# Performance work log

Hardware: AMD Instinct MI355X
Metric: run time of the kernel (lower is better)

## Reference

```python
import jax, jax.numpy as jnp
import numpy as np

N, E, B = 10000, 20000, 400
ND, ED, D = 32, 16, 64


def setup_inputs() -> dict:
    key = jax.random.key(0)
    ks = jax.random.split(key, 32)

    def lin(k, out_d, in_d):
        kw, kb = jax.random.split(k)
        s = 1.0 / np.sqrt(in_d)
        return (jax.random.uniform(kw, (out_d, in_d), jnp.float32, -s, s),
                jax.random.uniform(kb, (out_d,), jnp.float32, -s, s))

    W_in, b_in = lin(ks[0], D, ND)
    W_e1, b_e1 = lin(ks[1], D, ED)
    W_e2, b_e2 = lin(ks[2], D * D, D)
    b_conv = jax.random.uniform(ks[3], (D,), jnp.float32, -1/8.0, 1/8.0)
    W_ih, b_ih = lin(ks[4], 3 * D, D)
    W_hh, b_hh = lin(ks[5], 3 * D, D)
    W_ih_l, b_ih_l = lin(ks[6], 4 * D, 2 * D)
    W_hh_l, b_hh_l = lin(ks[7], 4 * D, D)
    W_o1, b_o1 = lin(ks[8], D, 2 * D)
    W_o2, b_o2 = lin(ks[9], 1, D)

    x = jax.random.normal(ks[10], (N, ND), jnp.float32)
    edge_attr = jax.random.normal(ks[11], (E, ED), jnp.float32)
    edge_index = jax.random.randint(ks[12], (2, E), 0, N, jnp.int64)
    batch = jnp.sort(jax.random.randint(ks[13], (N,), 0, B, jnp.int64))

    return dict(x=x, edge_attr=edge_attr,
                W_in=W_in, b_in=b_in, W_e1=W_e1, b_e1=b_e1, W_e2=W_e2, b_e2=b_e2,
                b_conv=b_conv, W_ih=W_ih, b_ih=b_ih, W_hh=W_hh, b_hh=b_hh,
                W_ih_l=W_ih_l, b_ih_l=b_ih_l, W_hh_l=W_hh_l, b_hh_l=b_hh_l,
                W_o1=W_o1, b_o1=b_o1, W_o2=W_o2, b_o2=b_o2,
                edge_index=edge_index, batch=batch)


def reference(x, edge_attr, W_in, b_in, W_e1, b_e1, W_e2, b_e2, b_conv,
              W_ih, b_ih, W_hh, b_hh, W_ih_l, b_ih_l, W_hh_l, b_hh_l,
              W_o1, b_o1, W_o2, b_o2, edge_index, batch):
    src, dst = edge_index[0], edge_index[1]

    # in_linear
    out = jax.nn.relu(x @ W_in.T + b_in)            # [N, D]
    h = out                                          # GRU hidden (layer=1, seq=1)

    # edge-conditioned weights: MLP(edge_attr) -> [E, D, D]
    ew = (jax.nn.relu(edge_attr @ W_e1.T + b_e1) @ W_e2.T + b_e2).reshape(E, D, D)
    cnt = jnp.maximum(jax.ops.segment_sum(jnp.ones((E,), x.dtype), dst, N), 1.0)

    for _ in range(3):
        # NNConv: gather src nodes, per-edge matmul, scatter-mean to dst, + bias
        msg = jnp.einsum('ed,edf->ef', out[src], ew)                 # [E, D]
        agg = jax.ops.segment_sum(msg, dst, N) / cnt[:, None] + b_conv
        m = jax.nn.relu(agg)
        # GRU cell (torch gate order r, z, n)
        gi = m @ W_ih.T + b_ih
        gh = h @ W_hh.T + b_hh
        i_r, i_z, i_n = jnp.split(gi, 3, axis=-1)
        h_r, h_z, h_n = jnp.split(gh, 3, axis=-1)
        r = jax.nn.sigmoid(i_r + h_r)
        z = jax.nn.sigmoid(i_z + h_z)
        n = jnp.tanh(i_n + r * h_n)
        h = (1.0 - z) * n + z * h
        out = h

    # Set2Set pooling, processing_steps=3
    q_star = jnp.zeros((B, 2 * D), x.dtype)
    hl = jnp.zeros((B, D), x.dtype)
    cl = jnp.zeros((B, D), x.dtype)
    for _ in range(3):
        g = q_star @ W_ih_l.T + b_ih_l + hl @ W_hh_l.T + b_hh_l
        gi_, gf_, gg_, go_ = jnp.split(g, 4, axis=-1)   # torch order i,f,g,o
        cl = jax.nn.sigmoid(gf_) * cl + jax.nn.sigmoid(gi_) * jnp.tanh(gg_)
        hl = jax.nn.sigmoid(go_) * jnp.tanh(cl)
        q = hl                                           # [B, D]
        e = jnp.sum(out * q[batch], axis=-1)             # [N]
        mmax = jax.ops.segment_max(e, batch, B)
        a = jnp.exp(e - mmax[batch])
        a = a / jax.ops.segment_sum(a, batch, B)[batch]
        r_ = jax.ops.segment_sum(a[:, None] * out, batch, B)  # [B, D]
        q_star = jnp.concatenate([q, r_], axis=-1)

    o = jax.nn.relu(q_star @ W_o1.T + b_o1) @ W_o2.T + b_o2
    return o.reshape(-1)
```

## Files before the change

### kernel.cpp

```cpp
#include <hip/hip_runtime.h>
#include <math.h>


#define Nn 10000
#define Ee 20000
#define Bb 400
#define KSTEPS 130
#define S2S_CHUNK 1024

#define FILL_A (Nn * 64)
#define FILL_B (KSTEPS * 4096)
#define FILL_C (4 * 2 * 16 * 64 * 8)

typedef __attribute__((ext_vector_type(8))) short bf16x8_t;
typedef __attribute__((ext_vector_type(4))) float f32x4_t;

__device__ __forceinline__ float sigmoidf_(float x) { return 1.f / (1.f + expf(-x)); }

__device__ __forceinline__ void split8(const float* p, bf16x8_t& Ahi_, bf16x8_t& Alo_) {
    union { bf16x8_t v; unsigned u[4]; } hi, lo;
#pragma unroll
    for (int ii = 0; ii < 4; ++ii) {
        float pa = p[2 * ii], pb = p[2 * ii + 1];
        unsigned ua = __float_as_uint(pa), ub = __float_as_uint(pb);
        hi.u[ii] = (ua >> 16) | (ub & 0xFFFF0000u);
        float la = pa - __uint_as_float(ua & 0xFFFF0000u);
        float lb = pb - __uint_as_float(ub & 0xFFFF0000u);
        lo.u[ii] = (__float_as_uint(la) >> 16) | (__float_as_uint(lb) & 0xFFFF0000u);
    }
    Ahi_ = hi.v; Alo_ = lo.v;
}

__global__ __launch_bounds__(256) void k_fill(const float* __restrict__ x,
                                              const float* __restrict__ Win,
                                              const float* __restrict__ bin,
                                              const float* __restrict__ W2,
                                              const float* __restrict__ b2,
                                              const float* __restrict__ Wih,
                                              const float* __restrict__ Whh,
                                              float* __restrict__ out,
                                              unsigned short* __restrict__ Bfat,
                                              unsigned short* __restrict__ Wg) {
    int idx = blockIdx.x * 256 + threadIdx.x;
    if (idx < FILL_A) {
        int n = idx >> 6, j = idx & 63;
        const float* xr = x + n * 32;
        const float* w = Win + j * 32;
        float acc = bin[j];
#pragma unroll
        for (int k = 0; k < 32; ++k) acc += xr[k] * w[k];
        out[idx] = fmaxf(acc, 0.f);
        return;
    }
    idx -= FILL_A;
    if (idx < FILL_B) {
        int i  = idx & 7;
        int l  = (idx >> 3) & 63;
        int nq = (idx >> 9) & 3;
        int h  = (idx >> 11) & 1;
        int ks = idx >> 12;
        int kap = ks * 32 + (l >> 4) * 8 + i;
        int f = nq * 16 + (l & 15);
        float w;
        if (kap < 4096) {
            int q = kap >> 6, d = kap & 63;
            w = W2[(size_t)(d * 64 + f) * 64 + q];
        } else {
            int d = kap - 4096;
            w = b2[d * 64 + f];
        }
        unsigned u = __float_as_uint(w);
        unsigned short outv;
        if (h == 0) {
            outv = (unsigned short)(u >> 16);
        } else {
            float lo = w - __uint_as_float(u & 0xFFFF0000u);
            outv = (unsigned short)(__float_as_uint(lo) >> 16);
        }
        Bfat[idx] = outv;
        return;
    }
    idx -= FILL_B;
    if (idx < FILL_C) {
        int i  = idx & 7;
        int l  = (idx >> 3) & 63;
        int t  = (idx >> 9) & 15;
        int h  = (idx >> 13) & 1;
        int ks = idx >> 14;
        int k = ks * 32 + (l >> 4) * 8 + i;
        int u = t * 16 + (l & 15);
        int j = u & 63, part = u >> 6;
        float w = 0.f;
        if (part == 0) w = (k < 64) ? Wih[(size_t)j * 64 + k]          : Whh[(size_t)j * 64 + (k - 64)];
        if (part == 1) w = (k < 64) ? Wih[(size_t)(64 + j) * 64 + k]   : Whh[(size_t)(64 + j) * 64 + (k - 64)];
        if (part == 2) w = (k < 64) ? Wih[(size_t)(128 + j) * 64 + k]  : 0.f;
        if (part == 3) w = (k < 64) ? 0.f : Whh[(size_t)(128 + j) * 64 + (k - 64)];
        unsigned uu = __float_as_uint(w);
        unsigned short outv;
        if (h == 0) {
            outv = (unsigned short)(uu >> 16);
        } else {
            float lo = w - __uint_as_float(uu & 0xFFFF0000u);
            outv = (unsigned short)(__float_as_uint(lo) >> 16);
        }
        Wg[idx] = outv;
    }
}

__global__ __launch_bounds__(256) void k_edge_mlp1(const float* __restrict__ ea,
                                                   const float* __restrict__ W1,
                                                   const float* __restrict__ b1,
                                                   const int* __restrict__ epos,
                                                   float* __restrict__ eh) {
    int idx = blockIdx.x * 256 + threadIdx.x;
    if (idx >= Ee * 64) return;
    int e = idx >> 6, j = idx & 63;
    const float* ar = ea + e * 16;
    const float* w = W1 + j * 16;
    float acc = b1[j];
#pragma unroll
    for (int k = 0; k < 16; ++k) acc += ar[k] * w[k];
    eh[(size_t)epos[e] * 64 + j] = fmaxf(acc, 0.f);
}

__global__ __launch_bounds__(256) void k_prep_count(const int* __restrict__ ei,
                                                    const int* __restrict__ batch,
                                                    int* __restrict__ deg,
                                                    int* __restrict__ bcount) {
    int idx = blockIdx.x * 256 + threadIdx.x;
    if (idx < Ee) {
        atomicAdd(&deg[ei[Ee + idx]], 1);
    } else if (idx < Ee + Nn) {
        atomicAdd(&bcount[batch[idx - Ee]], 1);
    }
}

__global__ __launch_bounds__(256) void k_prep_scan(const int* __restrict__ deg,
                                                   const int* __restrict__ bcount,
                                                   int* __restrict__ rowptr,
                                                   int* __restrict__ wptr,
                                                   int* __restrict__ bstart) {
    if (blockIdx.x == 0) {
        __shared__ int part[256];
        int t = threadIdx.x;
        const int PER = (Nn + 255) / 256;
        int b0 = t * PER;
        int s = 0;
        for (int i = 0; i < PER; ++i) {
            int idx = b0 + i;
            if (idx < Nn) s += deg[idx];
        }
        part[t] = s;
        __syncthreads();
        for (int o = 1; o < 256; o <<= 1) {
            int u = (t >= o) ? part[t - o] : 0;
            __syncthreads();
            part[t] += u;
            __syncthreads();
        }
        int run = part[t] - s;
        for (int i = 0; i < PER; ++i) {
            int idx = b0 + i;
            if (idx < Nn) {
                rowptr[idx] = run;
                wptr[idx] = run;
                run += deg[idx];
            }
        }
        if (t == 255) rowptr[Nn] = run;
    } else if (threadIdx.x < 64) {
        int lane = threadIdx.x;
        const int PER = (Bb + 63) / 64;
        int base = lane * PER;
        int v[PER];
        int s = 0;
#pragma unroll
        for (int i = 0; i < PER; ++i) {
            int idx = base + i;
            int c = (idx < Bb) ? bcount[idx] : 0;
            v[i] = s;
            s += c;
        }
        int inc = s;
#pragma unroll
        for (int o = 1; o < 64; o <<= 1) {
            int t = __shfl_up(inc, o, 64);
            if (lane >= o) inc += t;
        }
        int excl = inc - s;
        int total = __shfl(inc, 63, 64);
#pragma unroll
        for (int i = 0; i < PER; ++i) {
            int idx = base + i;
            if (idx < Bb) bstart[idx] = excl + v[i];
        }
        if (lane == 63) bstart[Bb] = total;
    }
}

__global__ __launch_bounds__(256) void k_sort_edges(const int* __restrict__ ei,
                                                    int* __restrict__ wptr,
                                                    int* __restrict__ srcs,
                                                    int* __restrict__ epos) {
    int e = blockIdx.x * 256 + threadIdx.x;
    if (e >= Ee) return;
    int d = ei[Ee + e];
    int p = atomicAdd(&wptr[d], 1);
    srcs[p] = ei[e];
    epos[e] = p;
}

__global__ __launch_bounds__(256) void k_msg_mfma(const float* __restrict__ out,
                                                  const float* __restrict__ eh,
                                                  const unsigned short* __restrict__ Bfat,
                                                  const int* __restrict__ srcs_g,
                                                  float* __restrict__ msgbuf,
                                                  int nsplit) {
    __shared__ float ehs[128][20];
    __shared__ int srcs[128];
    int tid = threadIdx.x;
    int ebase = blockIdx.x * 128;
    int ksplit = blockIdx.y;

    int ks0 = (KSTEPS * ksplit) / nsplit;
    int ks1 = (KSTEPS * (ksplit + 1)) / nsplit;
    int q0 = ks0 >> 1;
    int qn = ((min(ks1, 128) - 1) >> 1) - q0 + 1;

    {
        int el = tid >> 1, seg = tid & 1;
        int eg = ebase + el;
        bool v = eg < Ee;
        if (seg == 0) srcs[el] = v ? srcs_g[eg] : 0;
        const float* erow = eh + (size_t)eg * 64;
        for (int j = seg; j < qn; j += 2)
            ehs[el][j] = v ? erow[q0 + j] : 0.f;
    }
    __syncthreads();

    int lane = tid & 63;
    int wtile = tid >> 6;
    int m16 = lane & 15;
    int g = lane >> 4;
    int erA = wtile * 32 + m16;
    int erB = erA + 16;

    float a0[2][8], a1[2][8];
    {
        const float* rA = out + (size_t)srcs[erA] * 64;
        const float* rB = out + (size_t)srcs[erB] * 64;
        float4 v0, v1;
        v0 = *(const float4*)(rA + g * 8);      v1 = *(const float4*)(rA + g * 8 + 4);
        a0[0][0]=v0.x; a0[0][1]=v0.y; a0[0][2]=v0.z; a0[0][3]=v0.w;
        a0[0][4]=v1.x; a0[0][5]=v1.y; a0[0][6]=v1.z; a0[0][7]=v1.w;
        v0 = *(const float4*)(rA + 32 + g * 8); v1 = *(const float4*)(rA + 36 + g * 8);
        a1[0][0]=v0.x; a1[0][1]=v0.y; a1[0][2]=v0.z; a1[0][3]=v0.w;
        a1[0][4]=v1.x; a1[0][5]=v1.y; a1[0][6]=v1.z; a1[0][7]=v1.w;
        v0 = *(const float4*)(rB + g * 8);      v1 = *(const float4*)(rB + g * 8 + 4);
        a0[1][0]=v0.x; a0[1][1]=v0.y; a0[1][2]=v0.z; a0[1][3]=v0.w;
        a0[1][4]=v1.x; a0[1][5]=v1.y; a0[1][6]=v1.z; a0[1][7]=v1.w;
        v0 = *(const float4*)(rB + 32 + g * 8); v1 = *(const float4*)(rB + 36 + g * 8);
        a1[1][0]=v0.x; a1[1][1]=v0.y; a1[1][2]=v0.z; a1[1][3]=v0.w;
        a1[1][4]=v1.x; a1[1][5]=v1.y; a1[1][6]=v1.z; a1[1][7]=v1.w;
    }

    f32x4_t acc[2][4];
#pragma unroll
    for (int t = 0; t < 2; ++t)
#pragma unroll
        for (int nq = 0; nq < 4; ++nq) acc[t][nq] = (f32x4_t){0.f, 0.f, 0.f, 0.f};

    auto loadB = [&](int ks, bf16x8_t (&bh)[4], bf16x8_t (&bl)[4]) {
        const unsigned short* bstep = Bfat + (size_t)ks * 4096;
#pragma unroll
        for (int nq = 0; nq < 4; ++nq) {
            bh[nq] = *(const bf16x8_t*)(bstep + ((size_t)(nq * 64 + lane)) * 8);
            bl[nq] = *(const bf16x8_t*)(bstep + ((size_t)((4 + nq) * 64 + lane)) * 8);
        }
    };
    auto compute = [&](const float (&Av)[2][8], float qA, float qB,
                       const bf16x8_t (&bh)[4], const bf16x8_t (&bl)[4]) {
        float pA[8], pB[8];
#pragma unroll
        for (int i = 0; i < 8; ++i) { pA[i] = Av[0][i] * qA; pB[i] = Av[1][i] * qB; }
        bf16x8_t AhiA, AloA, AhiB, AloB;
        split8(pA, AhiA, AloA);
        split8(pB, AhiB, AloB);
#pragma unroll
        for (int nq = 0; nq < 4; ++nq) {
            acc[0][nq] = __builtin_amdgcn_mfma_f32_16x16x32_bf16(AhiA, bh[nq], acc[0][nq], 0, 0, 0);
            acc[0][nq] = __builtin_amdgcn_mfma_f32_16x16x32_bf16(AhiA, bl[nq], acc[0][nq], 0, 0, 0);
            acc[0][nq] = __builtin_amdgcn_mfma_f32_16x16x32_bf16(AloA, bh[nq], acc[0][nq], 0, 0, 0);
            acc[1][nq] = __builtin_amdgcn_mfma_f32_16x16x32_bf16(AhiB, bh[nq], acc[1][nq], 0, 0, 0);
            acc[1][nq] = __builtin_amdgcn_mfma_f32_16x16x32_bf16(AhiB, bl[nq], acc[1][nq], 0, 0, 0);
            acc[1][nq] = __builtin_amdgcn_mfma_f32_16x16x32_bf16(AloB, bh[nq], acc[1][nq], 0, 0, 0);
        }
    };

    bf16x8_t bEh[4], bEl[4], bOh[4], bOl[4];
    int kp0 = ks0 & ~1;
    loadB(kp0, bEh, bEl);
    for (int kp = kp0; kp < ks1; kp += 2) {
        bool hasOdd = (kp + 1 < ks1);
        if (hasOdd) loadB(kp + 1, bOh, bOl);
        float qA = 1.f, qB = 1.f;
        if (kp < 128) {
            int qi = (kp >> 1) - q0;
            if (qi >= 0) { qA = ehs[erA][qi]; qB = ehs[erB][qi]; }
        }
        if (kp >= ks0) compute(a0, qA, qB, bEh, bEl);
        if (kp + 2 < ks1) loadB(kp + 2, bEh, bEl);
        if (hasOdd) compute(a1, qA, qB, bOh, bOl);
    }

#pragma unroll
    for (int t = 0; t < 2; ++t) {
#pragma unroll
        for (int r = 0; r < 4; ++r) {
            int el = wtile * 32 + t * 16 + g * 4 + r;
            int eg = ebase + el;
            if (eg >= Ee) continue;
            float* mrow = msgbuf + ((size_t)ksplit * Ee + eg) * 64 + m16;
#pragma unroll
            for (int nq = 0; nq < 4; ++nq)
                mrow[nq * 16] = acc[t][nq][r];
        }
    }
}

__global__ __launch_bounds__(256) void k_gru_mfma(const float* __restrict__ msgbuf,
                                                  const int* __restrict__ rowptr,
                                                  const float* __restrict__ bconv,
                                                  const unsigned short* __restrict__ Wg,
                                                  const float* __restrict__ bih,
                                                  const float* __restrict__ bhh,
                                                  float* __restrict__ out,
                                                  int nsplit) {
    __shared__ float ms[64][68];
    __shared__ float hs[64][68];
    int tid = threadIdx.x;
    int nbase = blockIdx.x * 64;

    {
        int nl = tid >> 2, seg = tid & 3;
        int ng = nbase + nl;
        bool v = ng < Nn;
        int p0 = v ? rowptr[ng] : 0;
        int p1 = v ? rowptr[ng + 1] : 0;
        int dg = p1 - p0;
        float rc = 1.f / (float)(dg < 1 ? 1 : dg);
        float s[16];
#pragma unroll
        for (int i = 0; i < 16; ++i) s[i] = 0.f;
        for (int sp = 0; sp < nsplit; ++sp) {
            const float* mb = msgbuf + (size_t)sp * Ee * 64;
            for (int p = p0; p < p1; ++p) {
                const float* mrow = mb + (size_t)p * 64 + seg * 16;
#pragma unroll
                for (int c4 = 0; c4 < 4; ++c4) {
                    float4 t4 = *(const float4*)(mrow + c4 * 4);
                    s[c4 * 4 + 0] += t4.x;
                    s[c4 * 4 + 1] += t4.y;
                    s[c4 * 4 + 2] += t4.z;
                    s[c4 * 4 + 3] += t4.w;
                }
            }
        }
        const float* hrow = out + (size_t)ng * 64 + seg * 16;
        float4 z = make_float4(0.f, 0.f, 0.f, 0.f);
#pragma unroll
        for (int c4 = 0; c4 < 4; ++c4) {
            int col = seg * 16 + c4 * 4;
            float4 hv = v ? *(const float4*)(hrow + c4 * 4) : z;
            ms[nl][col + 0] = fmaxf(s[c4 * 4 + 0] * rc + bconv[col + 0], 0.f);
            ms[nl][col + 1] = fmaxf(s[c4 * 4 + 1] * rc + bconv[col + 1], 0.f);
            ms[nl][col + 2] = fmaxf(s[c4 * 4 + 2] * rc + bconv[col + 2], 0.f);
            ms[nl][col + 3] = fmaxf(s[c4 * 4 + 3] * rc + bconv[col + 3], 0.f);
            *(float4*)&hs[nl][col] = hv;
        }
    }
    __syncthreads();

    int lane = tid & 63;
    int wtile = tid >> 6;
    int m16 = lane & 15;
    int g = lane >> 4;
    int er = wtile * 16 + m16;

    f32x4_t acc[16];
#pragma unroll
    for (int t = 0; t < 16; ++t) acc[t] = (f32x4_t){0.f, 0.f, 0.f, 0.f};

#pragma unroll
    for (int ks = 0; ks < 4; ++ks) {
        const float* src = (ks < 2) ? &ms[er][ks * 32 + g * 8]
                                    : &hs[er][(ks - 2) * 32 + g * 8];
        float p[8];
#pragma unroll
        for (int ii = 0; ii < 8; ++ii) p[ii] = src[ii];
        bf16x8_t Ahi, Alo;
        split8(p, Ahi, Alo);
        const unsigned short* bstep = Wg + (size_t)ks * (2 * 16 * 512);
#pragma unroll
        for (int t = 0; t < 16; ++t) {
            bf16x8_t bhi = *(const bf16x8_t*)(bstep + ((size_t)t * 64 + lane) * 8);
            bf16x8_t blo = *(const bf16x8_t*)(bstep + ((size_t)(16 + t) * 64 + lane) * 8);
            acc[t] = __builtin_amdgcn_mfma_f32_16x16x32_bf16(Ahi, bhi, acc[t], 0, 0, 0);
            acc[t] = __builtin_amdgcn_mfma_f32_16x16x32_bf16(Ahi, blo, acc[t], 0, 0, 0);
            acc[t] = __builtin_amdgcn_mfma_f32_16x16x32_bf16(Alo, bhi, acc[t], 0, 0, 0);
        }
    }

#pragma unroll
    for (int t2 = 0; t2 < 4; ++t2) {
        int jj = t2 * 16 + m16;
        float br = bih[jj] + bhh[jj];
        float bz = bih[64 + jj] + bhh[64 + jj];
        float bin_ = bih[128 + jj];
        float bhn = bhh[128 + jj];
#pragma unroll
        for (int r = 0; r < 4; ++r) {
            int nl2 = wtile * 16 + g * 4 + r;
            int ng2 = nbase + nl2;
            if (ng2 >= Nn) continue;
            float rg = sigmoidf_(acc[t2][r] + br);
            float z  = sigmoidf_(acc[4 + t2][r] + bz);
            float nn = tanhf(acc[8 + t2][r] + bin_ + rg * (acc[12 + t2][r] + bhn));
            float hv = hs[nl2][jj];
            out[(size_t)ng2 * 64 + jj] = (1.f - z) * nn + z * hv;
        }
    }
}

__device__ __forceinline__ float block_reduce_max_(float v, float* red, int tid) {
#pragma unroll
    for (int o = 32; o; o >>= 1) v = fmaxf(v, __shfl_xor(v, o, 64));
    if ((tid & 63) == 0) red[tid >> 6] = v;
    __syncthreads();
    float r = fmaxf(fmaxf(red[0], red[1]), fmaxf(red[2], red[3]));
    __syncthreads();
    return r;
}
__device__ __forceinline__ float block_reduce_sum_(float v, float* red, int tid) {
#pragma unroll
    for (int o = 32; o; o >>= 1) v += __shfl_xor(v, o, 64);
    if ((tid & 63) == 0) red[tid >> 6] = v;
    __syncthreads();
    float r = (red[0] + red[1]) + (red[2] + red[3]);
    __syncthreads();
    return r;
}

__global__ __launch_bounds__(256) void k_set2set(const float* __restrict__ out,
                                                 const int* __restrict__ bstart,
                                                 const float* __restrict__ Wil,
                                                 const float* __restrict__ bil,
                                                 const float* __restrict__ Whl,
                                                 const float* __restrict__ bhl,
                                                 const float* __restrict__ Wo1,
                                                 const float* __restrict__ bo1,
                                                 const float* __restrict__ Wo2,
                                                 const float* __restrict__ bo2,
                                                 float* __restrict__ outp) {
    __shared__ float qs[128];
    __shared__ float hs2[64];
    __shared__ float cs[64];
    __shared__ float g_lds[256];
    __shared__ float e_lds[S2S_CHUNK];
    __shared__ float red[4];
    __shared__ float rpart[4][64];

    int b = blockIdx.x, tid = threadIdx.x;
    int lane = tid & 63, wv = tid >> 6;
    int s = bstart[b], eend = bstart[b + 1];
    int cntb = eend - s;

    if (tid < 128) qs[tid] = 0.f;
    if (tid < 64) { hs2[tid] = 0.f; cs[tid] = 0.f; }
    __syncthreads();

    for (int step = 0; step < 3; ++step) {
        {
            int u = tid;
            float acc = bil[u] + bhl[u];
            const float4* wi = (const float4*)(Wil + (size_t)u * 128);
#pragma unroll
            for (int k4 = 0; k4 < 32; ++k4) {
                float4 w = wi[k4];
                acc += qs[k4 * 4 + 0] * w.x + qs[k4 * 4 + 1] * w.y +
                       qs[k4 * 4 + 2] * w.z + qs[k4 * 4 + 3] * w.w;
            }
            const float4* wh = (const float4*)(Whl + (size_t)u * 64);
#pragma unroll
            for (int k4 = 0; k4 < 16; ++k4) {
                float4 w = wh[k4];
                acc += hs2[k4 * 4 + 0] * w.x + hs2[k4 * 4 + 1] * w.y +
                       hs2[k4 * 4 + 2] * w.z + hs2[k4 * 4 + 3] * w.w;
            }
            g_lds[u] = acc;
        }
        __syncthreads();
        if (tid < 64) {
            float c = sigmoidf_(g_lds[64 + tid]) * cs[tid] +
                      sigmoidf_(g_lds[tid]) * tanhf(g_lds[128 + tid]);
            cs[tid] = c;
            float h = sigmoidf_(g_lds[192 + tid]) * tanhf(c);
            hs2[tid] = h;
            qs[tid] = h;
        }
        __syncthreads();

        float gmax = -INFINITY, gsum = 0.f, racc = 0.f;
        for (int c0 = s; c0 < eend; c0 += S2S_CHUNK) {
            int clen = min(S2S_CHUNK, eend - c0);
            for (int i = tid; i < clen; i += 256) {
                const float4* orow = (const float4*)(out + (size_t)(c0 + i) * 64);
                float a0 = 0.f, a1 = 0.f, a2 = 0.f, a3 = 0.f;
#pragma unroll
                for (int k4 = 0; k4 < 16; k4 += 4) {
                    float4 o0 = orow[k4], o1 = orow[k4 + 1], o2 = orow[k4 + 2], o3 = orow[k4 + 3];
                    a0 += o0.x * qs[k4 * 4 + 0]  + o0.y * qs[k4 * 4 + 1]  + o0.z * qs[k4 * 4 + 2]  + o0.w * qs[k4 * 4 + 3];
                    a1 += o1.x * qs[k4 * 4 + 4]  + o1.y * qs[k4 * 4 + 5]  + o1.z * qs[k4 * 4 + 6]  + o1.w * qs[k4 * 4 + 7];
                    a2 += o2.x * qs[k4 * 4 + 8]  + o2.y * qs[k4 * 4 + 9]  + o2.z * qs[k4 * 4 + 10] + o2.w * qs[k4 * 4 + 11];
                    a3 += o3.x * qs[k4 * 4 + 12] + o3.y * qs[k4 * 4 + 13] + o3.z * qs[k4 * 4 + 14] + o3.w * qs[k4 * 4 + 15];
                }
                e_lds[i] = (a0 + a1) + (a2 + a3);
            }
            __syncthreads();
            float m = -INFINITY;
            for (int i = tid; i < clen; i += 256) m = fmaxf(m, e_lds[i]);
            float cmax = block_reduce_max_(m, red, tid);
            float nm = fmaxf(gmax, cmax);
            float scale = expf(gmax - nm);
            gsum *= scale; racc *= scale;
            float lsum = 0.f;
            for (int i = tid; i < clen; i += 256) {
                float av = expf(e_lds[i] - nm);
                e_lds[i] = av;
                lsum += av;
            }
            gsum += block_reduce_sum_(lsum, red, tid);
            for (int i = wv; i < clen; i += 4)
                racc += e_lds[i] * out[(size_t)(c0 + i) * 64 + lane];
            gmax = nm;
            __syncthreads();
        }
        rpart[wv][lane] = racc;
        __syncthreads();
        if (tid < 64) {
            float r = (rpart[0][tid] + rpart[1][tid]) + (rpart[2][tid] + rpart[3][tid]);
            qs[64 + tid] = (cntb > 0) ? r / gsum : 0.f;
        }
        __syncthreads();
    }

    if (tid < 64) {
        float acc = bo1[tid];
        const float4* w = (const float4*)(Wo1 + (size_t)tid * 128);
#pragma unroll
        for (int k4 = 0; k4 < 32; ++k4) {
            float4 wv4 = w[k4];
            acc += qs[k4 * 4 + 0] * wv4.x + qs[k4 * 4 + 1] * wv4.y +
                   qs[k4 * 4 + 2] * wv4.z + qs[k4 * 4 + 3] * wv4.w;
        }
        acc = fmaxf(acc, 0.f);
        float t = acc * Wo2[tid];
#pragma unroll
        for (int o = 32; o; o >>= 1) t += __shfl_xor(t, o, 64);
        if (tid == 0) outp[b] = t + bo2[0];
    }
}

extern "C" void kernel_launch(void* const* d_in, const int* in_sizes, int n_in,
                              void* d_out, int out_size, void* d_ws, size_t ws_size,
                              hipStream_t stream) {
    const float* x        = (const float*)d_in[0];
    const float* ea       = (const float*)d_in[1];
    const float* W_in     = (const float*)d_in[2];
    const float* b_in     = (const float*)d_in[3];
    const float* W_e1     = (const float*)d_in[4];
    const float* b_e1     = (const float*)d_in[5];
    const float* W_e2     = (const float*)d_in[6];
    const float* b_e2     = (const float*)d_in[7];
    const float* b_conv   = (const float*)d_in[8];
    const float* W_ih     = (const float*)d_in[9];
    const float* b_ih     = (const float*)d_in[10];
    const float* W_hh     = (const float*)d_in[11];
    const float* b_hh     = (const float*)d_in[12];
    const float* W_ih_l   = (const float*)d_in[13];
    const float* b_ih_l   = (const float*)d_in[14];
    const float* W_hh_l   = (const float*)d_in[15];
    const float* b_hh_l   = (const float*)d_in[16];
    const float* W_o1     = (const float*)d_in[17];
    const float* b_o1     = (const float*)d_in[18];
    const float* W_o2     = (const float*)d_in[19];
    const float* b_o2     = (const float*)d_in[20];
    const int*   ei       = (const int*)d_in[21];
    const int*   batch    = (const int*)d_in[22];
    float* outp = (float*)d_out;

    char* base = (char*)d_ws;
    size_t off = 0;
    auto carve = [&](size_t bytes) -> void* {
        void* p = base + off;
        off = (off + bytes + 255) & ~(size_t)255;
        return p;
    };

    int ns = 4;
    float *out, *msgbuf, *eh;
    unsigned short *Bfat, *Wg;
    int *srcs, *epos, *rowptr, *wptr, *deg, *bcount, *bstart;
    for (;; ns >>= 1) {
        off = 0;
        out    = (float*)carve((size_t)Nn * 64 * 4);
        msgbuf = (float*)carve((size_t)ns * Ee * 64 * 4);
        eh     = (float*)carve((size_t)Ee * 64 * 4);
        Bfat   = (unsigned short*)carve((size_t)KSTEPS * 4096 * 2);
        Wg     = (unsigned short*)carve((size_t)4 * 2 * 16 * 64 * 8 * 2);
        srcs   = (int*)carve((size_t)Ee * 4);
        epos   = (int*)carve((size_t)Ee * 4);
        rowptr = (int*)carve((size_t)(Nn + 1) * 4);
        wptr   = (int*)carve((size_t)Nn * 4);
        deg    = (int*)carve((size_t)Nn * 4);
        bcount = (int*)carve((size_t)Bb * 4);
        bstart = (int*)carve((size_t)(Bb + 1) * 4);
        if (off <= ws_size || ns == 1) break;
    }
    if (off > ws_size) return;

    hipMemsetAsync(deg, 0, (size_t)Nn * 4, stream);
    hipMemsetAsync(bcount, 0, (size_t)Bb * 4, stream);

    k_prep_count<<<(Ee + Nn + 255) / 256, 256, 0, stream>>>(ei, batch, deg, bcount);
    k_prep_scan<<<2, 256, 0, stream>>>(deg, bcount, rowptr, wptr, bstart);
    k_sort_edges<<<(Ee + 255) / 256, 256, 0, stream>>>(ei, wptr, srcs, epos);

    k_fill<<<(FILL_A + FILL_B + FILL_C + 255) / 256, 256, 0, stream>>>(
        x, W_in, b_in, W_e2, b_e2, W_ih, W_hh, out, Bfat, Wg);
    k_edge_mlp1<<<(Ee * 64) / 256, 256, 0, stream>>>(ea, W_e1, b_e1, epos, eh);

    int eblocks = (Ee + 127) / 128;
    int nblocks = (Nn + 63) / 64;
    for (int it = 0; it < 3; ++it) {
        k_msg_mfma<<<dim3(eblocks, ns), 256, 0, stream>>>(out, eh, Bfat, srcs, msgbuf, ns);
        k_gru_mfma<<<nblocks, 256, 0, stream>>>(msgbuf, rowptr, b_conv, Wg, b_ih, b_hh, out, ns);
    }

    k_set2set<<<Bb, 256, 0, stream>>>(out, bstart, W_ih_l, b_ih_l, W_hh_l, b_hh_l,
                                      W_o1, b_o1, W_o2, b_o2, outp);
}
```

Measured before the change: 332.8 us.

## Apply per-edge scale after MFMA and give each wave 64 edges

Measured after the change: 413.1 us. +24.1%, slower.

```diff
diff --git a/kernel.cpp b/kernel.cpp
--- a/kernel.cpp
+++ b/kernel.cpp
@@ -210,13 +210,13 @@
     epos[e] = p;
 }
 
-__global__ __launch_bounds__(256) void k_msg_mfma(const float* __restrict__ out,
+__global__ __launch_bounds__(128) void k_msg_mfma(const float* __restrict__ out,
                                                   const float* __restrict__ eh,
                                                   const unsigned short* __restrict__ Bfat,
                                                   const int* __restrict__ srcs_g,
                                                   float* __restrict__ msgbuf,
                                                   int nsplit) {
-    __shared__ float ehs[128][20];
+    __shared__ float ehs_t[17][128];
     __shared__ int srcs[128];
     int tid = threadIdx.x;
     int ebase = blockIdx.x * 128;
@@ -228,13 +228,12 @@
     int qn = ((min(ks1, 128) - 1) >> 1) - q0 + 1;
 
     {
-        int el = tid >> 1, seg = tid & 1;
-        int eg = ebase + el;
+        int eg = ebase + tid;
         bool v = eg < Ee;
-        if (seg == 0) srcs[el] = v ? srcs_g[eg] : 0;
-        const float* erow = eh + (size_t)eg * 64;
-        for (int j = seg; j < qn; j += 2)
-            ehs[el][j] = v ? erow[q0 + j] : 0.f;
+        srcs[tid] = v ? srcs_g[eg] : 0;
+        const float* erow = eh + (size_t)eg * 64 + q0;
+        for (int j = 0; j < qn; ++j)
+            ehs_t[j][tid] = v ? erow[j] : 0.f;
     }
     __syncthreads();
 
@@ -242,31 +241,28 @@
     int wtile = tid >> 6;
     int m16 = lane & 15;
     int g = lane >> 4;
-    int erA = wtile * 32 + m16;
-    int erB = erA + 16;
-
-    float a0[2][8], a1[2][8];
-    {
-        const float* rA = out + (size_t)srcs[erA] * 64;
-        const float* rB = out + (size_t)srcs[erB] * 64;
-        float4 v0, v1;
-        v0 = *(const float4*)(rA + g * 8);      v1 = *(const float4*)(rA + g * 8 + 4);
-        a0[0][0]=v0.x; a0[0][1]=v0.y; a0[0][2]=v0.z; a0[0][3]=v0.w;
-        a0[0][4]=v1.x; a0[0][5]=v1.y; a0[0][6]=v1.z; a0[0][7]=v1.w;
-        v0 = *(const float4*)(rA + 32 + g * 8); v1 = *(const float4*)(rA + 36 + g * 8);
-        a1[0][0]=v0.x; a1[0][1]=v0.y; a1[0][2]=v0.z; a1[0][3]=v0.w;
-        a1[0][4]=v1.x; a1[0][5]=v1.y; a1[0][6]=v1.z; a1[0][7]=v1.w;
-        v0 = *(const float4*)(rB + g * 8);      v1 = *(const float4*)(rB + g * 8 + 4);
-        a0[1][0]=v0.x; a0[1][1]=v0.y; a0[1][2]=v0.z; a0[1][3]=v0.w;
-        a0[1][4]=v1.x; a0[1][5]=v1.y; a0[1][6]=v1.z; a0[1][7]=v1.w;
-        v0 = *(const float4*)(rB + 32 + g * 8); v1 = *(const float4*)(rB + 36 + g * 8);
-        a1[1][0]=v0.x; a1[1][1]=v0.y; a1[1][2]=v0.z; a1[1][3]=v0.w;
-        a1[1][4]=v1.x; a1[1][5]=v1.y; a1[1][6]=v1.z; a1[1][7]=v1.w;
-    }
-
-    f32x4_t acc[2][4];
-#pragma unroll
-    for (int t = 0; t < 2; ++t)
+    int wbase = wtile * 64;
+
+    bf16x8_t A0h[4], A0l[4], A1h[4], A1l[4];
+#pragma unroll
+    for (int t = 0; t < 4; ++t) {
+        const float* r = out + (size_t)srcs[wbase + t * 16 + m16] * 64;
+        float a0[8], a1[8];
+        float4 v0 = *(const float4*)(r + g * 8);
+        float4 v1 = *(const float4*)(r + g * 8 + 4);
+        a0[0]=v0.x; a0[1]=v0.y; a0[2]=v0.z; a0[3]=v0.w;
+        a0[4]=v1.x; a0[5]=v1.y; a0[6]=v1.z; a0[7]=v1.w;
+        v0 = *(const float4*)(r + 32 + g * 8);
+        v1 = *(const float4*)(r + 36 + g * 8);
+        a1[0]=v0.x; a1[1]=v0.y; a1[2]=v0.z; a1[3]=v0.w;
+        a1[4]=v1.x; a1[5]=v1.y; a1[6]=v1.z; a1[7]=v1.w;
+        split8(a0, A0h[t], A0l[t]);
+        split8(a1, A1h[t], A1l[t]);
+    }
+
+    f32x4_t acc[4][4];
+#pragma unroll
+    for (int t = 0; t < 4; ++t)
 #pragma unroll
         for (int nq = 0; nq < 4; ++nq) acc[t][nq] = (f32x4_t){0.f, 0.f, 0.f, 0.f};
 
@@ -278,22 +274,26 @@
             bl[nq] = *(const bf16x8_t*)(bstep + ((size_t)((4 + nq) * 64 + lane)) * 8);
         }
     };
-    auto compute = [&](const float (&Av)[2][8], float qA, float qB,
-                       const bf16x8_t (&bh)[4], const bf16x8_t (&bl)[4]) {
-        float pA[8], pB[8];
-#pragma unroll
-        for (int i = 0; i < 8; ++i) { pA[i] = Av[0][i] * qA; pB[i] = Av[1][i] * qB; }
-        bf16x8_t AhiA, AloA, AhiB, AloB;
-        split8(pA, AhiA, AloA);
-        split8(pB, AhiB, AloB);
-#pragma unroll
-        for (int nq = 0; nq < 4; ++nq) {
-            acc[0][nq] = __builtin_amdgcn_mfma_f32_16x16x32_bf16(AhiA, bh[nq], acc[0][nq], 0, 0, 0);
-            acc[0][nq] = __builtin_amdgcn_mfma_f32_16x16x32_bf16(AhiA, bl[nq], acc[0][nq], 0, 0, 0);
-            acc[0][nq] = __builtin_amdgcn_mfma_f32_16x16x32_bf16(AloA, bh[nq], acc[0][nq], 0, 0, 0);
-            acc[1][nq] = __builtin_amdgcn_mfma_f32_16x16x32_bf16(AhiB, bh[nq], acc[1][nq], 0, 0, 0);
-            acc[1][nq] = __builtin_amdgcn_mfma_f32_16x16x32_bf16(AhiB, bl[nq], acc[1][nq], 0, 0, 0);
-            acc[1][nq] = __builtin_amdgcn_mfma_f32_16x16x32_bf16(AloB, bh[nq], acc[1][nq], 0, 0, 0);
+    auto computeP = [&](int kp, const bf16x8_t (&Ah)[4], const bf16x8_t (&Al)[4],
+                        const bf16x8_t (&bh)[4], const bf16x8_t (&bl)[4]) {
+#pragma unroll
+        for (int t = 0; t < 4; ++t) {
+            float q0v = 1.f, q1v = 1.f, q2v = 1.f, q3v = 1.f;
+            if (kp < 128) {
+                float4 q4 = *(const float4*)&ehs_t[(kp >> 1) - q0][wbase + t * 16 + g * 4];
+                q0v = q4.x; q1v = q4.y; q2v = q4.z; q3v = q4.w;
+            }
+#pragma unroll
+            for (int nq = 0; nq < 4; ++nq) {
+                f32x4_t U = (f32x4_t){0.f, 0.f, 0.f, 0.f};
+                U = __builtin_amdgcn_mfma_f32_16x16x32_bf16(Al[t], bh[nq], U, 0, 0, 0);
+                U = __builtin_amdgcn_mfma_f32_16x16x32_bf16(Ah[t], bl[nq], U, 0, 0, 0);
+                U = __builtin_amdgcn_mfma_f32_16x16x32_bf16(Ah[t], bh[nq], U, 0, 0, 0);
+                acc[t][nq][0] += q0v * U[0];
+                acc[t][nq][1] += q1v * U[1];
+                acc[t][nq][2] += q2v * U[2];
+                acc[t][nq][3] += q3v * U[3];
+            }
         }
     };
 
@@ -303,21 +303,16 @@
     for (int kp = kp0; kp < ks1; kp += 2) {
         bool hasOdd = (kp + 1 < ks1);
         if (hasOdd) loadB(kp + 1, bOh, bOl);
-        float qA = 1.f, qB = 1.f;
-        if (kp < 128) {
-            int qi = (kp >> 1) - q0;
-            if (qi >= 0) { qA = ehs[erA][qi]; qB = ehs[erB][qi]; }
-        }
-        if (kp >= ks0) compute(a0, qA, qB, bEh, bEl);
+        if (kp >= ks0) computeP(kp, A0h, A0l, bEh, bEl);
         if (kp + 2 < ks1) loadB(kp + 2, bEh, bEl);
-        if (hasOdd) compute(a1, qA, qB, bOh, bOl);
-    }
-
-#pragma unroll
-    for (int t = 0; t < 2; ++t) {
+        if (hasOdd) computeP(kp + 1, A1h, A1l, bOh, bOl);
+    }
+
+#pragma unroll
+    for (int t = 0; t < 4; ++t) {
 #pragma unroll
         for (int r = 0; r < 4; ++r) {
-            int el = wtile * 32 + t * 16 + g * 4 + r;
+            int el = wbase + t * 16 + g * 4 + r;
             int eg = ebase + el;
             if (eg >= Ee) continue;
             float* mrow = msgbuf + ((size_t)ksplit * Ee + eg) * 64 + m16;
@@ -643,7 +638,7 @@
     int eblocks = (Ee + 127) / 128;
     int nblocks = (Nn + 63) / 64;
     for (int it = 0; it < 3; ++it) {
-        k_msg_mfma<<<dim3(eblocks, ns), 256, 0, stream>>>(out, eh, Bfat, srcs, msgbuf, ns);
+        k_msg_mfma<<<dim3(eblocks, ns), 128, 0, stream>>>(out, eh, Bfat, srcs, msgbuf, ns);
         k_gru_mfma<<<nblocks, 256, 0, stream>>>(msgbuf, rowptr, b_conv, Wg, b_ih, b_hh, out, ns);
     }
 
```
